# Optimization experiments

Measured on AMD Instinct MI355X. Metric: run time of the kernel, lower is better.

The kernel has to match this reference:

```python
import jax, jax.numpy as jnp
import numpy as np

R, C, B, E, H = 16, 256, 12, 768, 12  # rows, cols, batch(==heads, see notes), embed, heads
D = E // H
NUM_BUCKETS, MAX_DISTANCE = 32, 50000


def _relative_position_bucket(distances):
    # T5-style log-spaced buckets, matching the torch code (trunc toward zero).
    n = jnp.abs(distances)
    max_exact = NUM_BUCKETS // 2
    is_small = n < max_exact
    nf = jnp.maximum(n.astype(jnp.float32), 1.0)  # guard log(0); masked by is_small
    val_large = max_exact + (
        jnp.log(nf / max_exact) / np.log(MAX_DISTANCE / max_exact) * (NUM_BUCKETS - max_exact - 1)
    ).astype(jnp.int32)
    val_large = jnp.minimum(val_large, NUM_BUCKETS - 1)
    return jnp.where(is_small, n.astype(jnp.int32), val_large)


def setup_inputs() -> dict:
    key = jax.random.key(0)
    ks = jax.random.split(key, 11)
    s = 1.0 / np.sqrt(E)
    x = jax.random.normal(ks[0], (R, C, B, E), jnp.float32)
    distances = jax.random.randint(ks[1], (B, C, C), 0, MAX_DISTANCE, jnp.int32)
    Wq = jax.random.normal(ks[2], (E, E), jnp.float32) * s
    bq = jnp.zeros((E,), jnp.float32)
    Wk = jax.random.normal(ks[3], (E, E), jnp.float32) * s
    bk = jnp.zeros((E,), jnp.float32)
    Wv = jax.random.normal(ks[4], (E, E), jnp.float32) * s
    bv = jnp.zeros((E,), jnp.float32)
    Wo = jax.random.normal(ks[5], (E, E), jnp.float32) * s
    bo = jnp.zeros((E,), jnp.float32)
    rel_bias = jax.random.normal(ks[6], (NUM_BUCKETS, H), jnp.float32) * 0.02
    return dict(x=x, distances=distances, Wq=Wq, bq=bq, Wk=Wk, bk=bk,
                Wv=Wv, bv=bv, Wo=Wo, bo=bo, rel_bias=rel_bias)


def reference(x, distances, Wq, bq, Wk, bk, Wv, bv, Wo, bo, rel_bias):
    scaling = (D ** -0.5) / np.sqrt(R)  # align_scaling: head_dim^-0.5 / sqrt(num_rows)
    q = (x @ Wq.T + bq).reshape(R, C, B, H, D) * scaling
    k = (x @ Wk.T + bk).reshape(R, C, B, H, D)
    # row-aggregated scores: sum over rows r -> (h, n, i, j)
    attn = jnp.einsum('rinhd,rjnhd->hnij', q, k)
    # relative position bias: (n, i, j) -> buckets -> (n, i, j, h) -> (n, h, i, j)
    buckets = _relative_position_bucket(distances)
    bias = jnp.transpose(rel_bias[buckets], (0, 3, 1, 2))
    # NOTE: source adds (n,h,i,j) bias onto (h,n,i,j) scores positionally; valid since B == H.
    attn = attn + bias
    probs = jax.nn.softmax(attn, axis=-1)  # (h, n, i, j)
    v = (x @ Wv.T + bv).reshape(R, C, B, H, D)
    ctx = jnp.einsum('hnij,rjnhd->rinhd', probs, v).reshape(R, C, B, E)
    out = ctx @ Wo.T + bo
    return out, probs
```

## Files before the change

kernel.cpp:

```cpp
#include <hip/hip_runtime.h>
#include <stdint.h>
#include <math.h>

#define R_ 16
#define C_ 256
#define B_ 12
#define E_ 768
#define H_ 12
#define D_ 64
#define TOK (R_*C_*B_)

#define VT_N_ELEMS 3145728
#define CTX_N_ELEMS 3145728
#define QK_HALF 37748736

typedef __bf16 bf16x8 __attribute__((ext_vector_type(8)));
typedef float floatx4 __attribute__((ext_vector_type(4)));

__device__ __forceinline__ unsigned short f2bf(float f) {
    union { unsigned int i; float f; } v; v.f = f;
    unsigned int i = v.i;
    return (unsigned short)((i + 0x7fffu + ((i >> 16) & 1u)) >> 16);
}
__device__ __forceinline__ bf16x8 cvt8(floatx4 lo, floatx4 hi) {
    bf16x8 r;
    r[0] = (__bf16)lo[0]; r[1] = (__bf16)lo[1]; r[2] = (__bf16)lo[2]; r[3] = (__bf16)lo[3];
    r[4] = (__bf16)hi[0]; r[5] = (__bf16)hi[1]; r[6] = (__bf16)hi[2]; r[7] = (__bf16)hi[3];
    return r;
}
__device__ __forceinline__ void gload16(const unsigned short* g, unsigned short* l) {
    __builtin_amdgcn_global_load_lds(
        (const __attribute__((address_space(1))) unsigned int*)g,
        (__attribute__((address_space(3))) unsigned int*)l, 16, 0, 0);
}

template<int MODE>
__global__ __launch_bounds__(256)
void gemm_bt(const void* __restrict__ Ap,
             const void* __restrict__ Btp,
             const float* __restrict__ bias,
             void* __restrict__ Cout,
             int nBase)
{
    constexpr bool AGL = (MODE == 1 || MODE == 4);
    constexpr int K = (MODE == 1) ? 1024 : ((MODE == 2) ? 256 : 768);
    constexpr int kIters = K >> 5;
    constexpr int GX = (MODE==0) ? 12 : (MODE==1) ? 2 : (MODE==2) ? 8 : 6;
    constexpr int GY = (MODE==0) ? 384 : (MODE==1) ? 2 : (MODE==2) ? 2 : 32;
    constexpr int GZ = (MODE==0) ? 1 : (MODE==1) ? 144 : (MODE==2) ? 24 : 2;

    __shared__ __align__(16) unsigned short As[128 * 32];
    __shared__ __align__(16) unsigned short Bs[128 * 32];

    const int tid  = threadIdx.x;
    const int wave = tid >> 6, lane = tid & 63;
    const int quad = lane >> 4, l15 = lane & 15;
    const int wr = wave >> 1, wc = wave & 1;

    const int lin = ((int)blockIdx.z * GY + (int)blockIdx.y) * GX + (int)blockIdx.x;
    const int tt  = (lin & 7) * ((GX * GY * GZ) >> 3) + (lin >> 3);
    const int bx  = tt % GX;
    const int rem = tt / GX;
    const int by  = rem % GY, bz = rem / GY;
    const int row0 = by * 128, col0 = bx * 128;

    int hIdx = 0, nn = 0, nIdx = 0;
    if (MODE == 1) { hIdx = bz % 12; nIdx = bz / 12; }
    if (MODE == 2) { hIdx = bz % 12; nn = bz / 12; nIdx = nBase + nn; }
    if (MODE == 3 || MODE == 4) { nn = bz; nIdx = nBase + nn; }

    const int rA0 = tid >> 2;
    const int ck  = tid & 3;
    const int sw  = (tid >> 3) & 3;
    const int kko = ((ck ^ sw) << 3);

    const unsigned short* Bt = (const unsigned short*)Btp;
    const unsigned short *gB0, *gB1;
    if (MODE == 1) {
        gB0 = Bt + ((size_t)bz * 256 + col0 + rA0) * 1024 + kko;
        gB1 = Bt + ((size_t)bz * 256 + col0 + rA0 + 64) * 1024 + kko;
    } else if (MODE == 2) {
        gB0 = Bt + (((size_t)nn * 12 + hIdx) * 1024 + col0 + rA0) * 256 + kko;
        gB1 = Bt + (((size_t)nn * 12 + hIdx) * 1024 + col0 + rA0 + 64) * 256 + kko;
    } else {
        gB0 = Bt + (size_t)(col0 + rA0) * 768 + kko;
        gB1 = Bt + (size_t)(col0 + rA0 + 64) * 768 + kko;
    }

    const unsigned short* gA0u = nullptr; const unsigned short* gA1u = nullptr;
    const float* gA0f = nullptr; const float* gA1f = nullptr;
    if (MODE == 1) {
        gA0u = (const unsigned short*)Ap + ((size_t)bz * 256 + row0 + rA0) * 1024 + kko;
        gA1u = (const unsigned short*)Ap + ((size_t)bz * 256 + row0 + rA0 + 64) * 1024 + kko;
    } else if (MODE == 4) {
        gA0u = (const unsigned short*)Ap + (size_t)nn * CTX_N_ELEMS
               + (size_t)(row0 + rA0) * 768 + kko;
        gA1u = (const unsigned short*)Ap + (size_t)nn * CTX_N_ELEMS
               + (size_t)(row0 + rA0 + 64) * 768 + kko;
    } else if (MODE == 0) {
        gA0f = (const float*)Ap + (size_t)(row0 + rA0) * 768 + kko;
        gA1f = (const float*)Ap + (size_t)(row0 + rA0 + 64) * 768 + kko;
    } else if (MODE == 3) {
        gA0f = (const float*)Ap + ((size_t)(row0 + rA0) * 12 + nIdx) * 768 + kko;
        gA1f = (const float*)Ap + ((size_t)(row0 + rA0 + 64) * 12 + nIdx) * 768 + kko;
    } else {
        gA0f = (const float*)Ap + ((size_t)(hIdx * 12 + nIdx)) * 65536
               + (size_t)(row0 + rA0) * 256 + kko;
        gA1f = (const float*)Ap + ((size_t)(hIdx * 12 + nIdx)) * 65536
               + (size_t)(row0 + rA0 + 64) * 256 + kko;
    }

    unsigned short* lA0 = As + wave * 512;
    unsigned short* lA1 = As + 2048 + wave * 512;
    unsigned short* lB0 = Bs + wave * 512;
    unsigned short* lB1 = Bs + 2048 + wave * 512;

    const floatx4 zero = {0.f, 0.f, 0.f, 0.f};
    floatx4 acc[4][4];
#pragma unroll
    for (int i = 0; i < 4; ++i)
#pragma unroll
        for (int j = 0; j < 4; ++j) acc[i][j] = zero;

    const int chO = ((quad ^ ((l15 >> 1) & 3)) << 3);

    floatx4 u0l = zero, u0h = zero, u1l = zero, u1h = zero;
    floatx4 p0l = zero, p0h = zero, p1l = zero, p1h = zero;
    if (!AGL) {
        u0l = *(const floatx4*)(gA0f);     u0h = *(const floatx4*)(gA0f + 4);
        u1l = *(const floatx4*)(gA1f);     u1h = *(const floatx4*)(gA1f + 4);
    }

#define GSTEP(KT, UL0, UH0, UL1, UH1, PL0, PH0, PL1, PH1)                         \
    {                                                                              \
        __syncthreads();             \
        gload16(gB0 + (KT) * 32, lB0);                                             \
        gload16(gB1 + (KT) * 32, lB1);                                             \
        if (AGL) {                                                                 \
            gload16(gA0u + (KT) * 32, lA0);                                        \
            gload16(gA1u + (KT) * 32, lA1);                                        \
        } else {                                                                   \
            *(bf16x8*)(As + tid * 8)        = cvt8(UL0, UH0);                      \
            *(bf16x8*)(As + 2048 + tid * 8) = cvt8(UL1, UH1);                      \
        }                                                                          \
        __syncthreads();        \
        if (!AGL && ((KT) + 1 < kIters)) {             \
            PL0 = *(const floatx4*)(gA0f + ((KT) + 1) * 32);                       \
            PH0 = *(const floatx4*)(gA0f + ((KT) + 1) * 32 + 4);                   \
            PL1 = *(const floatx4*)(gA1f + ((KT) + 1) * 32);                       \
            PH1 = *(const floatx4*)(gA1f + ((KT) + 1) * 32 + 4);                   \
        }                                                                          \
        bf16x8 af[4], bfr[4];                                                      \
        _Pragma("unroll")                                                          \
        for (int t = 0; t < 4; ++t) {                                              \
            af[t]  = *(const bf16x8*)(As + (wr * 64 + t * 16 + l15) * 32 + chO);   \
            bfr[t] = *(const bf16x8*)(Bs + (wc * 64 + t * 16 + l15) * 32 + chO);   \
        }                                                                          \
        _Pragma("unroll")                                                          \
        for (int tm = 0; tm < 4; ++tm)                                             \
            _Pragma("unroll")                                                      \
            for (int tn = 0; tn < 4; ++tn)                                         \
                acc[tm][tn] = __builtin_amdgcn_mfma_f32_16x16x32_bf16(             \
                    af[tm], bfr[tn], acc[tm][tn], 0, 0, 0);                        \
    }

    for (int kt = 0; kt < kIters; kt += 2) {
        GSTEP(kt,     u0l, u0h, u1l, u1h, p0l, p0h, p1l, p1h);
        GSTEP(kt + 1, p0l, p0h, p1l, p1h, u0l, u0h, u1l, u1h);
    }
#undef GSTEP

#pragma unroll
    for (int tm = 0; tm < 4; ++tm) {
        const int rbase = row0 + wr * 64 + tm * 16 + quad * 4;
#pragma unroll
        for (int tn = 0; tn < 4; ++tn) {
            const int cc = col0 + wc * 64 + tn * 16 + l15;
#pragma unroll
            for (int rr = 0; rr < 4; ++rr) {
                float vv = acc[tm][tn][rr];
                const int rowg = rbase + rr;
                if (MODE == 0) {
                    const int m = rowg / 12, n = rowg - m * 12;
                    const int r = m >> 8, i = m & 255;
                    const int sel = cc >= 768 ? 1 : 0;
                    const int ccl = cc - sel * 768;
                    const int h = ccl >> 6, d = ccl & 63;
                    ((unsigned short*)Cout)[(size_t)sel * QK_HALF
                        + ((size_t)(n * 12 + h) * 256 + i) * 1024 + r * 64 + d]
                        = f2bf(vv + bias[cc]);
                } else if (MODE == 1) {
                    ((float*)Cout)[((size_t)(hIdx * 12 + nIdx)) * 65536
                                   + (size_t)rowg * 256 + cc] = vv * 0.03125f;
                } else if (MODE == 2) {
                    ((unsigned short*)Cout)[(size_t)nn * CTX_N_ELEMS
                        + (((size_t)(cc >> 6)) * 256 + rowg) * 768
                        + hIdx * 64 + (cc & 63)] = f2bf(vv);
                } else if (MODE == 3) {
                    ((unsigned short*)Cout)[(size_t)nn * VT_N_ELEMS
                        + (((size_t)(cc >> 6)) * 1024
                           + (rowg >> 8) * 64 + (cc & 63)) * 256
                        + (rowg & 255)] = f2bf(vv + bias[cc]);
                } else {
                    ((float*)Cout)[((size_t)rowg * 12 + nIdx) * 768 + cc] = vv + bias[cc];
                }
            }
        }
    }
}

__global__ __launch_bounds__(256)
void cvt_w(const float* __restrict__ src, unsigned short* __restrict__ dst, int n)
{
    const int i = (blockIdx.x * 256 + threadIdx.x) * 8;
    if (i >= n) return;
    floatx4 a = ((const floatx4*)(src + i))[0];
    floatx4 b = ((const floatx4*)(src + i))[1];
    *(bf16x8*)(dst + i) = cvt8(a, b);
}

__global__ __launch_bounds__(256)
void bucket_kernel(const int* __restrict__ dist, int* __restrict__ buckets)
{
    const int idx = blockIdx.x * 256 + threadIdx.x;
    if (idx >= B_ * C_ * C_) return;
    const int dv = dist[idx];
    const int n = dv < 0 ? -dv : dv;
    int bkt;
    if (n < 16) {
        bkt = n;
    } else {
        const float lg = logf((float)n * 0.0625f);
        const float t  = (lg / 8.047189562170502f) * 15.0f;
        bkt = 16 + (int)t;
        if (bkt > 31) bkt = 31;
    }
    buckets[idx] = bkt;
}

__global__ __launch_bounds__(256)
void softmax_bias(float* __restrict__ probs,
                  const int* __restrict__ buckets,
                  const float* __restrict__ rb)
{
    const int wave = threadIdx.x >> 6, lane = threadIdx.x & 63;
    const int rowid = blockIdx.x * 4 + wave;
    const int p = rowid >> 8;
    const int i = rowid & 255;
    const int a = p / 12, b = p - a * 12;
    float* prow = probs + (size_t)rowid * 256;
    const int* brow = buckets + ((size_t)a * 256 + i) * 256;

    float vals[4];
    float mx = -3.4e38f;
#pragma unroll
    for (int t = 0; t < 4; ++t) {
        const int j = t * 64 + lane;
        vals[t] = prow[j] + rb[brow[j] * 12 + b];
        mx = fmaxf(mx, vals[t]);
    }
#pragma unroll
    for (int off = 32; off > 0; off >>= 1) mx = fmaxf(mx, __shfl_xor(mx, off, 64));
    float sum = 0.f;
#pragma unroll
    for (int t = 0; t < 4; ++t) { vals[t] = expf(vals[t] - mx); sum += vals[t]; }
#pragma unroll
    for (int off = 32; off > 0; off >>= 1) sum += __shfl_xor(sum, off, 64);
    const float inv = 1.f / sum;
#pragma unroll
    for (int t = 0; t < 4; ++t) prow[t * 64 + lane] = vals[t] * inv;
}

extern "C" void kernel_launch(void* const* d_in, const int* in_sizes, int n_in,
                              void* d_out, int out_size, void* d_ws, size_t ws_size,
                              hipStream_t stream)
{
    const float* x    = (const float*)d_in[0];
    const int*   dist = (const int*)d_in[1];
    const float* Wq   = (const float*)d_in[2];
    const float* bq   = (const float*)d_in[3];
    const float* Wk   = (const float*)d_in[4];
    const float* bk   = (const float*)d_in[5];
    const float* Wv   = (const float*)d_in[6];
    const float* bv   = (const float*)d_in[7];
    const float* Wo   = (const float*)d_in[8];
    const float* bo   = (const float*)d_in[9];
    const float* rb   = (const float*)d_in[10];

    float* outp  = (float*)d_out;
    float* probs = (float*)d_out + (size_t)TOK * E_;

    unsigned short* qs = (unsigned short*)d_out;
    unsigned short* ks = (unsigned short*)d_out + QK_HALF;

    char* ws = (char*)d_ws;
    unsigned short* wv_bf  = (unsigned short*)(ws);
    unsigned short* wo_bf  = (unsigned short*)(ws + 1179648);
    float*          bqk    = (float*)(ws + 2359296);
    unsigned short* wqk_bf = (unsigned short*)(ws + 2365440);
    int*            buckets= (int*)(ws + 4724736);
    unsigned short* vt     = (unsigned short*)(ws + 2365440);
    unsigned short* ctx    = (unsigned short*)(ws + 14948352);

    dim3 blk(256);

    cvt_w<<<dim3(288), blk, 0, stream>>>(Wq, wqk_bf, 589824);
    cvt_w<<<dim3(288), blk, 0, stream>>>(Wk, wqk_bf + 589824, 589824);
    cvt_w<<<dim3(288), blk, 0, stream>>>(Wv, wv_bf, 589824);
    cvt_w<<<dim3(288), blk, 0, stream>>>(Wo, wo_bf, 589824);
    hipMemcpyAsync(bqk,       bq, 768 * 4, hipMemcpyDeviceToDevice, stream);
    hipMemcpyAsync(bqk + 768, bk, 768 * 4, hipMemcpyDeviceToDevice, stream);

    bucket_kernel<<<dim3(3072), blk, 0, stream>>>(dist, buckets);

    gemm_bt<0><<<dim3(12, 384), blk, 0, stream>>>(x, wqk_bf, bqk, qs, 0);
    gemm_bt<1><<<dim3(2, 2, 144), blk, 0, stream>>>(qs, ks, nullptr, probs, 0);

    softmax_bias<<<dim3(9216), blk, 0, stream>>>(probs, buckets, rb);

    for (int c = 0; c < 6; ++c) {
        const int n0 = 2 * c;
        gemm_bt<3><<<dim3(6, 32, 2), blk, 0, stream>>>(x, wv_bf, bv, vt, n0);
        gemm_bt<2><<<dim3(8, 2, 24), blk, 0, stream>>>(probs, vt, nullptr, ctx, n0);
        gemm_bt<4><<<dim3(6, 32, 2), blk, 0, stream>>>(ctx, wo_bf, bo, outp, n0);
    }
}
```

Baseline: 973.8 us.

## Pre-convert x to bf16, fuse weight casts, and overlap V/O projections across chunks

```diff
diff --git a/kernel.cpp b/kernel.cpp
--- a/kernel.cpp
+++ b/kernel.cpp
@@ -9,6 +9,7 @@
 #define H_ 12
 #define D_ 64
 #define TOK (R_*C_*B_)
+#define HALF_TOK 24576
 
 #define VT_N_ELEMS 3145728
 #define CTX_N_ELEMS 3145728
@@ -35,29 +36,26 @@
 }
 
 template<int MODE>
-__global__ __launch_bounds__(256)
-void gemm_bt(const void* __restrict__ Ap,
-             const void* __restrict__ Btp,
-             const float* __restrict__ bias,
-             void* __restrict__ Cout,
-             int nBase)
-{
-    constexpr bool AGL = (MODE == 1 || MODE == 4);
+__device__ __forceinline__ void gemm_body(const void* __restrict__ Ap,
+                                          const void* __restrict__ Btp,
+                                          const float* __restrict__ bias,
+                                          void* __restrict__ Cout,
+                                          int nBase, int rbx, int rby, int rbz,
+                                          unsigned short* As, unsigned short* Bs)
+{
+    constexpr bool AGL = (MODE == 0 || MODE == 1 || MODE == 4);
     constexpr int K = (MODE == 1) ? 1024 : ((MODE == 2) ? 256 : 768);
     constexpr int kIters = K >> 5;
     constexpr int GX = (MODE==0) ? 12 : (MODE==1) ? 2 : (MODE==2) ? 8 : 6;
-    constexpr int GY = (MODE==0) ? 384 : (MODE==1) ? 2 : (MODE==2) ? 2 : 32;
+    constexpr int GY = (MODE==0) ? 192 : (MODE==1) ? 2 : (MODE==2) ? 2 : 32;
     constexpr int GZ = (MODE==0) ? 1 : (MODE==1) ? 144 : (MODE==2) ? 24 : 2;
-
-    __shared__ __align__(16) unsigned short As[128 * 32];
-    __shared__ __align__(16) unsigned short Bs[128 * 32];
 
     const int tid  = threadIdx.x;
     const int wave = tid >> 6, lane = tid & 63;
     const int quad = lane >> 4, l15 = lane & 15;
     const int wr = wave >> 1, wc = wave & 1;
 
-    const int lin = ((int)blockIdx.z * GY + (int)blockIdx.y) * GX + (int)blockIdx.x;
+    const int lin = (rbz * GY + rby) * GX + rbx;
     const int tt  = (lin & 7) * ((GX * GY * GZ) >> 3) + (lin >> 3);
     const int bx  = tt % GX;
     const int rem = tt / GX;
@@ -89,7 +87,10 @@
 
     const unsigned short* gA0u = nullptr; const unsigned short* gA1u = nullptr;
     const float* gA0f = nullptr; const float* gA1f = nullptr;
-    if (MODE == 1) {
+    if (MODE == 0) {
+        gA0u = (const unsigned short*)Ap + (size_t)(row0 + rA0) * 768 + kko;
+        gA1u = (const unsigned short*)Ap + (size_t)(row0 + rA0 + 64) * 768 + kko;
+    } else if (MODE == 1) {
         gA0u = (const unsigned short*)Ap + ((size_t)bz * 256 + row0 + rA0) * 1024 + kko;
         gA1u = (const unsigned short*)Ap + ((size_t)bz * 256 + row0 + rA0 + 64) * 1024 + kko;
     } else if (MODE == 4) {
@@ -97,9 +98,6 @@
                + (size_t)(row0 + rA0) * 768 + kko;
         gA1u = (const unsigned short*)Ap + (size_t)nn * CTX_N_ELEMS
                + (size_t)(row0 + rA0 + 64) * 768 + kko;
-    } else if (MODE == 0) {
-        gA0f = (const float*)Ap + (size_t)(row0 + rA0) * 768 + kko;
-        gA1f = (const float*)Ap + (size_t)(row0 + rA0 + 64) * 768 + kko;
     } else if (MODE == 3) {
         gA0f = (const float*)Ap + ((size_t)(row0 + rA0) * 12 + nIdx) * 768 + kko;
         gA1f = (const float*)Ap + ((size_t)(row0 + rA0 + 64) * 12 + nIdx) * 768 + kko;
@@ -133,7 +131,7 @@
 
 #define GSTEP(KT, UL0, UH0, UL1, UH1, PL0, PH0, PL1, PH1)                         \
     {                                                                              \
-        __syncthreads();             \
+        __syncthreads();                                \
         gload16(gB0 + (KT) * 32, lB0);                                             \
         gload16(gB1 + (KT) * 32, lB1);                                             \
         if (AGL) {                                                                 \
@@ -143,7 +141,7 @@
             *(bf16x8*)(As + tid * 8)        = cvt8(UL0, UH0);                      \
             *(bf16x8*)(As + 2048 + tid * 8) = cvt8(UL1, UH1);                      \
         }                                                                          \
-        __syncthreads();        \
+        __syncthreads();                                      \
         if (!AGL && ((KT) + 1 < kIters)) {             \
             PL0 = *(const floatx4*)(gA0f + ((KT) + 1) * 32);                       \
             PH0 = *(const floatx4*)(gA0f + ((KT) + 1) * 32 + 4);                   \
@@ -181,7 +179,8 @@
                 float vv = acc[tm][tn][rr];
                 const int rowg = rbase + rr;
                 if (MODE == 0) {
-                    const int m = rowg / 12, n = rowg - m * 12;
+                    const int tg = nBase * HALF_TOK + rowg;
+                    const int m = tg / 12, n = tg - m * 12;
                     const int r = m >> 8, i = m & 255;
                     const int sel = cc >= 768 ? 1 : 0;
                     const int ccl = cc - sel * 768;
@@ -209,14 +208,68 @@
     }
 }
 
-__global__ __launch_bounds__(256)
-void cvt_w(const float* __restrict__ src, unsigned short* __restrict__ dst, int n)
+template<int MODE>
+__global__ __launch_bounds__(256)
+void gemm_bt(const void* __restrict__ Ap,
+             const void* __restrict__ Btp,
+             const float* __restrict__ bias,
+             void* __restrict__ Cout,
+             int nBase)
+{
+    __shared__ __align__(16) unsigned short As[128 * 32];
+    __shared__ __align__(16) unsigned short Bs[128 * 32];
+    gemm_body<MODE>(Ap, Btp, bias, Cout, nBase,
+                    blockIdx.x, blockIdx.y, blockIdx.z, As, Bs);
+}
+
+__global__ __launch_bounds__(256)
+void fused_vo(const float* __restrict__ x, const unsigned short* __restrict__ wv,
+              const float* __restrict__ bv, unsigned short* __restrict__ vt,
+              const unsigned short* __restrict__ ctx,
+              const unsigned short* __restrict__ wo,
+              const float* __restrict__ bo, float* __restrict__ outp,
+              int cV, int cO)
+{
+    __shared__ __align__(16) unsigned short As[128 * 32];
+    __shared__ __align__(16) unsigned short Bs[128 * 32];
+    if (blockIdx.z < 2)
+        gemm_body<3>(x, wv, bv, vt, cV, blockIdx.x, blockIdx.y, blockIdx.z, As, Bs);
+    else
+        gemm_body<4>(ctx, wo, bo, outp, cO, blockIdx.x, blockIdx.y,
+                     blockIdx.z - 2, As, Bs);
+}
+
+__global__ __launch_bounds__(256)
+void cvt_bulk(const float* __restrict__ src, unsigned short* __restrict__ dst, int n)
 {
     const int i = (blockIdx.x * 256 + threadIdx.x) * 8;
     if (i >= n) return;
     floatx4 a = ((const floatx4*)(src + i))[0];
     floatx4 b = ((const floatx4*)(src + i))[1];
     *(bf16x8*)(dst + i) = cvt8(a, b);
+}
+
+__global__ __launch_bounds__(256)
+void cvt_weights(const float* __restrict__ Wq, const float* __restrict__ Wk,
+                 const float* __restrict__ Wv, const float* __restrict__ Wo,
+                 const float* __restrict__ bq, const float* __restrict__ bk,
+                 unsigned short* __restrict__ wqk, unsigned short* __restrict__ wvb,
+                 unsigned short* __restrict__ wob, float* __restrict__ bqk)
+{
+    const int gid = blockIdx.x * 256 + threadIdx.x;
+    const int W8 = 73728;
+    if (gid < 4 * W8) {
+        const int sec = gid / W8, off = (gid - sec * W8) * 8;
+        const float* src = (sec == 0) ? Wq : (sec == 1) ? Wk : (sec == 2) ? Wv : Wo;
+        unsigned short* dst = (sec == 0) ? wqk : (sec == 1) ? (wqk + 589824)
+                              : (sec == 2) ? wvb : wob;
+        floatx4 a = ((const floatx4*)(src + off))[0];
+        floatx4 b = ((const floatx4*)(src + off))[1];
+        *(bf16x8*)(dst + off) = cvt8(a, b);
+    } else {
+        const int b = gid - 4 * W8;
+        if (b < 1536) bqk[b] = (b < 768) ? bq[b] : bk[b - 768];
+    }
 }
 
 __global__ __launch_bounds__(256)
@@ -290,12 +343,12 @@
     float* outp  = (float*)d_out;
     float* probs = (float*)d_out + (size_t)TOK * E_;
 
-    unsigned short* qs = (unsigned short*)d_out;
-    unsigned short* ks = (unsigned short*)d_out + QK_HALF;
+    unsigned short* qs   = (unsigned short*)d_out;
+    unsigned short* x_bf = (unsigned short*)probs;
 
     char* ws = (char*)d_ws;
-    unsigned short* wv_bf  = (unsigned short*)(ws);
-    unsigned short* wo_bf  = (unsigned short*)(ws + 1179648);
+    unsigned short* wo_bf  = (unsigned short*)(ws);
+    unsigned short* wv_bf  = (unsigned short*)(ws + 1179648);
     float*          bqk    = (float*)(ws + 2359296);
     unsigned short* wqk_bf = (unsigned short*)(ws + 2365440);
     int*            buckets= (int*)(ws + 4724736);
@@ -304,24 +357,26 @@
 
     dim3 blk(256);
 
-    cvt_w<<<dim3(288), blk, 0, stream>>>(Wq, wqk_bf, 589824);
-    cvt_w<<<dim3(288), blk, 0, stream>>>(Wk, wqk_bf + 589824, 589824);
-    cvt_w<<<dim3(288), blk, 0, stream>>>(Wv, wv_bf, 589824);
-    cvt_w<<<dim3(288), blk, 0, stream>>>(Wo, wo_bf, 589824);
-    hipMemcpyAsync(bqk,       bq, 768 * 4, hipMemcpyDeviceToDevice, stream);
-    hipMemcpyAsync(bqk + 768, bk, 768 * 4, hipMemcpyDeviceToDevice, stream);
-
+    cvt_weights<<<dim3(1158), blk, 0, stream>>>(Wq, Wk, Wv, Wo, bq, bk,
+                                                wqk_bf, wv_bf, wo_bf, bqk);
     bucket_kernel<<<dim3(3072), blk, 0, stream>>>(dist, buckets);
 
-    gemm_bt<0><<<dim3(12, 384), blk, 0, stream>>>(x, wqk_bf, bqk, qs, 0);
-    gemm_bt<1><<<dim3(2, 2, 144), blk, 0, stream>>>(qs, ks, nullptr, probs, 0);
+    for (int half = 0; half < 2; ++half) {
+        cvt_bulk<<<dim3(9216), blk, 0, stream>>>(
+            x + (size_t)half * HALF_TOK * 768, x_bf, HALF_TOK * 768);
+        gemm_bt<0><<<dim3(12, 192), blk, 0, stream>>>(x_bf, wqk_bf, bqk, qs, half);
+    }
+    gemm_bt<1><<<dim3(2, 2, 144), blk, 0, stream>>>(
+        qs, (unsigned short*)d_out + QK_HALF, nullptr, probs, 0);
 
     softmax_bias<<<dim3(9216), blk, 0, stream>>>(probs, buckets, rb);
 
-    for (int c = 0; c < 6; ++c) {
-        const int n0 = 2 * c;
-        gemm_bt<3><<<dim3(6, 32, 2), blk, 0, stream>>>(x, wv_bf, bv, vt, n0);
-        gemm_bt<2><<<dim3(8, 2, 24), blk, 0, stream>>>(probs, vt, nullptr, ctx, n0);
-        gemm_bt<4><<<dim3(6, 32, 2), blk, 0, stream>>>(ctx, wo_bf, bo, outp, n0);
-    }
-}
+    gemm_bt<3><<<dim3(6, 32, 2), blk, 0, stream>>>(x, wv_bf, bv, vt, 0);
+    gemm_bt<2><<<dim3(8, 2, 24), blk, 0, stream>>>(probs, vt, nullptr, ctx, 0);
+    for (int k = 1; k < 6; ++k) {
+        fused_vo<<<dim3(6, 32, 4), blk, 0, stream>>>(
+            x, wv_bf, bv, vt, ctx, wo_bf, bo, outp, 2 * k, 2 * (k - 1));
+        gemm_bt<2><<<dim3(8, 2, 24), blk, 0, stream>>>(probs, vt, nullptr, ctx, 2 * k);
+    }
+    gemm_bt<4><<<dim3(6, 32, 2), blk, 0, stream>>>(ctx, wo_bf, bo, outp, 10);
+}
```

Result: faster. 873.3 us (-10.3%).
